# Performance work log

Measured on AMD Instinct MI355X. Metric: run time of the kernel, lower is better.

## Reference

```python
import jax, jax.numpy as jnp
import numpy as np

N_NODES = 50000
N_EDGES = 800000
IN_DIM = 128
ATT_DIM = 128
NEG_SLOPE = 0.01  # nn.LeakyReLU default


def setup_inputs() -> dict:
    key = jax.random.key(0)
    ks = jax.random.split(key, 8)
    x = jax.random.normal(ks[0], (N_NODES, IN_DIM), dtype=jnp.float32)
    src_idx = jax.random.randint(ks[1], (N_EDGES,), 0, N_NODES, dtype=jnp.int32)
    dst_idx = jax.random.randint(ks[2], (N_EDGES,), 0, N_NODES, dtype=jnp.int32)
    # small init scale keeps exp(score) numerically tame
    src_w = jax.random.normal(ks[3], (IN_DIM, ATT_DIM), dtype=jnp.float32) * 0.05
    src_b = jnp.zeros((ATT_DIM,), dtype=jnp.float32)
    dst_w = jax.random.normal(ks[4], (IN_DIM, ATT_DIM), dtype=jnp.float32) * 0.05
    dst_b = jnp.zeros((ATT_DIM,), dtype=jnp.float32)
    att_w = jax.random.normal(ks[5], (ATT_DIM, 1), dtype=jnp.float32) * 0.05
    att_b = jnp.zeros((1,), dtype=jnp.float32)
    return {"x": x, "src_idx": src_idx, "dst_idx": dst_idx,
            "src_w": src_w, "src_b": src_b, "dst_w": dst_w, "dst_b": dst_b,
            "att_w": att_w, "att_b": att_b}


def reference(x, src_idx, dst_idx, src_w, src_b, dst_w, dst_b, att_w, att_b):
    n = x.shape[0]
    # 1) mean aggregation of source features onto destinations (copy_u + mean)
    deg = jax.ops.segment_sum(jnp.ones_like(dst_idx, dtype=x.dtype), dst_idx, num_segments=n)
    h_mean = jax.ops.segment_sum(x[src_idx], dst_idx, num_segments=n)
    h_mean = h_mean / jnp.maximum(deg, 1.0)[:, None]
    # 2) attention projections on nodes (dense GEMMs)
    ha_src = x @ src_w + src_b          # [N, att_dim]
    ha_dst = h_mean @ dst_w + dst_b     # [N, att_dim]
    # 3) per-edge u_add_v -> LeakyReLU -> att Linear -> exp
    e = jax.nn.leaky_relu(ha_src[src_idx] + ha_dst[dst_idx], NEG_SLOPE)  # [E, att_dim]
    s = jnp.exp(e @ att_w + att_b)      # [E, 1]
    # 4) edge softmax: normalize by segment sum over destination
    denom = jax.ops.segment_sum(s, dst_idx, num_segments=n)  # [N, 1]
    a = s / denom[dst_idx]              # [E, 1]
    # 5) u_mul_e weighted aggregation (sum)
    out = jax.ops.segment_sum(x[src_idx] * a, dst_idx, num_segments=n)  # [N, in_dim]
    return out
```

## Files before the change

kernel.cpp:

```cpp
#include <hip/hip_runtime.h>
#include <math.h>

#define N_NODES 50000
#define N_EDGES 800000
#define DIM 128
#define NEG_SLOPE 0.01f
#define CAP 64
#define DEGS 32

#define GEMM_BLOCKS 3125
#define SCAT_BLOCKS 3125

typedef short v8s __attribute__((ext_vector_type(8)));
typedef float v4f __attribute__((ext_vector_type(4)));
typedef float v2f __attribute__((ext_vector_type(2)));

__device__ inline unsigned f2bf2(float a, float b) {
    unsigned ua = __float_as_uint(a);
    unsigned ub = __float_as_uint(b);
    ua = (ua + 0x7fffu + ((ua >> 16) & 1u)) >> 16;
    ub = (ub + 0x7fffu + ((ub >> 16) & 1u)) & 0xffff0000u;
    return ua | ub;
}
__device__ inline v2f bf2v(unsigned u) {
    v2f r;
    r.x = __uint_as_float(u << 16);
    r.y = __uint_as_float(u & 0xffff0000u);
    return r;
}
__device__ inline v2f lk2(v2f v) {
    return __builtin_elementwise_max(v, v * NEG_SLOPE);
}

#define ROR_ADD(v, CTRL) \
    ((v) + __int_as_float(__builtin_amdgcn_update_dpp( \
        0, __float_as_int(v), (CTRL), 0xf, 0xf, false)))

__global__ __launch_bounds__(256) void k_scatter(
    const int* __restrict__ src, const int* __restrict__ dst,
    int* __restrict__ deg, int* __restrict__ slots,
    const float* __restrict__ src_w, const float* __restrict__ dst_w,
    unsigned* __restrict__ whT)
{
    int bx = blockIdx.x;
    int tid = threadIdx.x;
    if (bx < 64) {
        int gid = bx * 256 + tid;
        int n = gid >> 6;
        int kk = gid & 63;
        const float* W = (n < 128) ? src_w : dst_w;
        int col = n & 127;
        float w0 = W[(2 * kk) * DIM + col];
        float w1 = W[(2 * kk + 1) * DIM + col];
        whT[gid] = f2bf2(w0, w1);
    }
    int e = bx * 256 + tid;
    int s = src[e];
    int d = dst[e];
    int pos = atomicAdd(&deg[d * DEGS], 1);
    if (pos < CAP) slots[d * CAP + pos] = s * 64;
}

__global__ __launch_bounds__(64) void k_gemm(
    const float* __restrict__ x, const unsigned* __restrict__ whT,
    const float* __restrict__ src_b, unsigned* __restrict__ hx_u,
    unsigned* __restrict__ yu)
{
    __shared__ unsigned L[16][132];
    int bx = blockIdx.x;
    int lane = threadIdx.x;
    int quad = lane >> 4;
    int m = lane & 15;

    int arow = bx * 16 + m;
    const float4* xp = (const float4*)(x + (size_t)arow * DIM + quad * 8);
    float4 f[4][2];
    #pragma unroll
    for (int k0 = 0; k0 < 4; ++k0) {
        f[k0][0] = xp[k0 * 8];
        f[k0][1] = xp[k0 * 8 + 1];
    }

    v8s b[4];
    #pragma unroll
    for (int k0 = 0; k0 < 4; ++k0) {
        union { unsigned u[4]; v8s s; } pk;
        pk.u[0] = f2bf2(f[k0][0].x, f[k0][0].y);
        pk.u[1] = f2bf2(f[k0][0].z, f[k0][0].w);
        pk.u[2] = f2bf2(f[k0][1].x, f[k0][1].y);
        pk.u[3] = f2bf2(f[k0][1].z, f[k0][1].w);
        b[k0] = pk.s;
        int c = k0 * 32 + quad * 8 + 1;
        L[m][c + 0] = pk.u[0];
        L[m][c + 2] = pk.u[1];
        L[m][c + 4] = pk.u[2];
        L[m][c + 6] = pk.u[3];
    }

    v4f yacc[8];
    #pragma unroll
    for (int nt = 0; nt < 16; ++nt) {
        v4f acc = {0.f, 0.f, 0.f, 0.f};
        const uint4* ap = (const uint4*)(whT + (size_t)(nt * 16 + m) * 64 + quad * 4);
        #pragma unroll
        for (int k0 = 0; k0 < 4; ++k0) {
            union { uint4 u; v8s s; } af;
            af.u = ap[k0 * 4];
            acc = __builtin_amdgcn_mfma_f32_16x16x32_bf16(af.s, b[k0], acc, 0, 0, 0);
        }
        if (nt < 8) {
            float4 bia = ((const float4*)src_b)[nt * 4 + quad];
            int c = nt * 16 + quad * 4;
            L[m][c]     = f2bf2(acc[0] + bia.x, acc[1] + bia.y);
            L[m][c + 2] = f2bf2(acc[2] + bia.z, acc[3] + bia.w);
        } else {
            yacc[nt - 8] = acc;
        }
    }

    int rbase0 = bx * 16;
    for (int i = lane; i < 512; i += 64) {
        int r = i >> 5, c = i & 31;
        ((uint4*)(hx_u + (size_t)(rbase0 + r) * 128))[c] = *(const uint4*)&L[r][c * 4];
    }

    #pragma unroll
    for (int t = 0; t < 8; ++t) {
        int c = t * 8 + quad * 2;
        L[m][c]     = f2bf2(yacc[t][0], yacc[t][1]);
        L[m][c + 1] = f2bf2(yacc[t][2], yacc[t][3]);
    }
    for (int i = lane; i < 256; i += 64) {
        int r = i >> 4, c = i & 15;
        ((uint4*)(yu + (size_t)(rbase0 + r) * 64))[c] = *(const uint4*)&L[r][c * 4];
    }
}

__global__ __launch_bounds__(256) void k_fuse(
    const uint2* __restrict__ hx, const unsigned* __restrict__ yu,
    const int* __restrict__ slots, const int* __restrict__ deg,
    const float* __restrict__ dst_b, const float* __restrict__ att_w,
    const float* __restrict__ att_b, float* __restrict__ out)
{
    int g = blockIdx.x * 256 + threadIdx.x;
    int node = g >> 6;
    int lane = g & 63;
    int grp = lane >> 4;
    int sl = lane & 15;
    int cnt = deg[node * DEGS];
    if (cnt == 0) {
        if (grp < 2) {
            v4f z = {0.f, 0.f, 0.f, 0.f};
            __builtin_nontemporal_store(z, (v4f*)out + node * 32 + (grp ? 16 + sl : sl));
        }
        return;
    }
    int cc = (cnt < CAP) ? cnt : CAP;
    int trips = (cc + 3) >> 2;
    int myoff = (lane < cc) ? slots[node * CAP + lane] : 0;

    v2f hd01 = {0.f, 0.f}, hd23 = {0.f, 0.f};
    v2f hd45 = {0.f, 0.f}, hd67 = {0.f, 0.f};
    #pragma unroll 4
    for (int t = 0; t < trips; ++t) {
        int i = 4 * t + grp;
        bool valid = (i < cc);
        int off = __shfl(myoff, valid ? i : 0);
        if (valid) {
            const uint2* yp = (const uint2*)(yu + off);
            uint2 qa = yp[sl];
            uint2 qb = yp[16 + sl];
            hd01 += bf2v(qa.x);
            hd23 += bf2v(qa.y);
            hd45 += bf2v(qb.x);
            hd67 += bf2v(qb.y);
        }
    }
    float inv = 1.0f / (float)cnt;
    float m0 = hd01.x, m1 = hd01.y, m2 = hd23.x, m3 = hd23.y;
    float m4 = hd45.x, m5 = hd45.y, m6 = hd67.x, m7 = hd67.y;
    #define XRED(f) { f += __shfl_xor(f, 32); f += __shfl_xor(f, 16); f *= inv; }
    XRED(m0) XRED(m1) XRED(m2) XRED(m3) XRED(m4) XRED(m5) XRED(m6) XRED(m7)
    #undef XRED
    float4 db0 = ((const float4*)dst_b)[sl];
    float4 db1 = ((const float4*)dst_b)[16 + sl];
    hd01 = (v2f){m0 + db0.x, m1 + db0.y};
    hd23 = (v2f){m2 + db0.z, m3 + db0.w};
    hd45 = (v2f){m4 + db1.x, m5 + db1.y};
    hd67 = (v2f){m6 + db1.z, m7 + db1.w};

    float4 aw0f = ((const float4*)att_w)[sl];
    float4 aw1f = ((const float4*)att_w)[16 + sl];
    v2f aw01 = (v2f){aw0f.x, aw0f.y}, aw23 = (v2f){aw0f.z, aw0f.w};
    v2f aw45 = (v2f){aw1f.x, aw1f.y}, aw67 = (v2f){aw1f.z, aw1f.w};
    float ab = att_b[0];
    v2f o01 = {0.f, 0.f}, o23 = {0.f, 0.f};
    v2f o45 = {0.f, 0.f}, o67 = {0.f, 0.f};
    float dsum = 0.f;
    #pragma unroll 4
    for (int t = 0; t < trips; ++t) {
        int i = 4 * t + grp;
        bool valid = (i < cc);
        int off = __shfl(myoff, valid ? i : 0);
        if (valid) {
            const uint4* hp = (const uint4*)(hx + off);
            uint4 qa = hp[sl];
            uint4 qb = hp[16 + sl];
            v2f p2 = {0.f, 0.f};
            p2 = __builtin_elementwise_fma(lk2(bf2v(qa.x) + hd01), aw01, p2);
            p2 = __builtin_elementwise_fma(lk2(bf2v(qa.z) + hd23), aw23, p2);
            p2 = __builtin_elementwise_fma(lk2(bf2v(qb.x) + hd45), aw45, p2);
            p2 = __builtin_elementwise_fma(lk2(bf2v(qb.z) + hd67), aw67, p2);
            float p = p2.x + p2.y;
            p = ROR_ADD(p, 0x128);
            p = ROR_ADD(p, 0x124);
            p = ROR_ADD(p, 0x122);
            p = ROR_ADD(p, 0x121);
            float s = __expf(p + ab);
            v2f s2 = (v2f){s, s};
            o01 = __builtin_elementwise_fma(bf2v(qa.y), s2, o01);
            o23 = __builtin_elementwise_fma(bf2v(qa.w), s2, o23);
            o45 = __builtin_elementwise_fma(bf2v(qb.y), s2, o45);
            o67 = __builtin_elementwise_fma(bf2v(qb.w), s2, o67);
            dsum += s;
        }
    }
    dsum += __shfl_xor(dsum, 32);
    dsum += __shfl_xor(dsum, 16);
    float r0 = o01.x, r1 = o01.y, r2 = o23.x, r3 = o23.y;
    float r4 = o45.x, r5 = o45.y, r6 = o67.x, r7 = o67.y;
    #define XRED2(f) { f += __shfl_xor(f, 32); f += __shfl_xor(f, 16); }
    XRED2(r0) XRED2(r1) XRED2(r2) XRED2(r3) XRED2(r4) XRED2(r5) XRED2(r6) XRED2(r7)
    #undef XRED2
    float r = 1.0f / dsum;
    if (grp < 2) {
        v4f ov;
        if (grp == 0) {
            ov[0] = r0 * r; ov[1] = r1 * r; ov[2] = r2 * r; ov[3] = r3 * r;
            __builtin_nontemporal_store(ov, (v4f*)out + node * 32 + sl);
        } else {
            ov[0] = r4 * r; ov[1] = r5 * r; ov[2] = r6 * r; ov[3] = r7 * r;
            __builtin_nontemporal_store(ov, (v4f*)out + node * 32 + 16 + sl);
        }
    }
}

extern "C" void kernel_launch(void* const* d_in, const int* in_sizes, int n_in,
                              void* d_out, int out_size, void* d_ws, size_t ws_size,
                              hipStream_t stream)
{
    const float* x     = (const float*)d_in[0];
    const int*   src   = (const int*)d_in[1];
    const int*   dst   = (const int*)d_in[2];
    const float* src_w = (const float*)d_in[3];
    const float* src_b = (const float*)d_in[4];
    const float* dst_w = (const float*)d_in[5];
    const float* dst_b = (const float*)d_in[6];
    const float* att_w = (const float*)d_in[7];
    const float* att_b = (const float*)d_in[8];
    float* out = (float*)d_out;
    (void)in_sizes; (void)n_in; (void)out_size; (void)ws_size;

    const size_t NF = (size_t)N_NODES * DIM;

    int* ws = (int*)d_ws;
    int* ideg  = ws;
    int* slots = ws + 1600512;
    unsigned* whT = (unsigned*)(ws + 4800512);
    unsigned* yu  = whT + 16384;
    uint2*    hx  = (uint2*)(yu + NF / 2);

    hipMemsetAsync(ideg, 0, (size_t)N_NODES * DEGS * sizeof(int), stream);

    k_scatter<<<SCAT_BLOCKS, 256, 0, stream>>>(
        src, dst, ideg, slots, src_w, dst_w, whT);

    k_gemm<<<GEMM_BLOCKS, 64, 0, stream>>>(x, whT, src_b, (unsigned*)hx, yu);

    k_fuse<<<N_NODES * 64 / 256, 256, 0, stream>>>(
        hx, yu, slots, ideg, dst_b, att_w, att_b, out);
}
```

Measured before the change: 246.8 us.

## Merge edge scatter into GEMM kernel and replace memset with prep kernel

Splits the weight transpose/bf16 pack into a small prep kernel that also zeroes the degree counters, which removes the hipMemsetAsync. The edge scatter and node GEMM now share one launch, with odd and even blocks interleaved so the atomic-heavy scatter overlaps the MFMA GEMM. Scatter blocks now run 64 threads handling 4 edges each. This saves a launch and lets the latency-bound atomics hide under compute, at the cost of smaller scatter blocks and a heterogeneous grid.

```diff
diff --git a/kernel.cpp b/kernel.cpp
--- a/kernel.cpp
+++ b/kernel.cpp
@@ -10,6 +10,7 @@
 
 #define GEMM_BLOCKS 3125
 #define SCAT_BLOCKS 3125
+#define MERGED_BLOCKS (GEMM_BLOCKS + SCAT_BLOCKS)
 
 typedef short v8s __attribute__((ext_vector_type(8)));
 typedef float v4f __attribute__((ext_vector_type(4)));
@@ -36,16 +37,12 @@
     ((v) + __int_as_float(__builtin_amdgcn_update_dpp( \
         0, __float_as_int(v), (CTRL), 0xf, 0xf, false)))
 
-__global__ __launch_bounds__(256) void k_scatter(
-    const int* __restrict__ src, const int* __restrict__ dst,
-    int* __restrict__ deg, int* __restrict__ slots,
+__global__ __launch_bounds__(256) void k_prepw(
     const float* __restrict__ src_w, const float* __restrict__ dst_w,
-    unsigned* __restrict__ whT)
-{
-    int bx = blockIdx.x;
-    int tid = threadIdx.x;
-    if (bx < 64) {
-        int gid = bx * 256 + tid;
+    unsigned* __restrict__ whT, int* __restrict__ deg)
+{
+    int gid = blockIdx.x * 256 + threadIdx.x;
+    if (gid < 256 * 64) {
         int n = gid >> 6;
         int kk = gid & 63;
         const float* W = (n < 128) ? src_w : dst_w;
@@ -54,21 +51,39 @@
         float w1 = W[(2 * kk + 1) * DIM + col];
         whT[gid] = f2bf2(w0, w1);
     }
-    int e = bx * 256 + tid;
-    int s = src[e];
-    int d = dst[e];
-    int pos = atomicAdd(&deg[d * DEGS], 1);
-    if (pos < CAP) slots[d * CAP + pos] = s * 64;
-}
-
-__global__ __launch_bounds__(64) void k_gemm(
+    if (gid < N_NODES) deg[gid * DEGS] = 0;
+}
+
+__global__ __launch_bounds__(64) void k_scatgemm(
+    const int* __restrict__ src, const int* __restrict__ dst,
+    int* __restrict__ deg, int* __restrict__ slots,
     const float* __restrict__ x, const unsigned* __restrict__ whT,
     const float* __restrict__ src_b, unsigned* __restrict__ hx_u,
     unsigned* __restrict__ yu)
 {
     __shared__ unsigned L[16][132];
-    int bx = blockIdx.x;
+    int b = blockIdx.x;
     int lane = threadIdx.x;
+
+    if (b & 1) {
+        int bs = b >> 1;
+        int e0 = bs * 256 + lane;
+        int sv[4], dv[4], pos[4];
+        #pragma unroll
+        for (int i = 0; i < 4; ++i) {
+            sv[i] = src[e0 + i * 64];
+            dv[i] = dst[e0 + i * 64];
+        }
+        #pragma unroll
+        for (int i = 0; i < 4; ++i)
+            pos[i] = atomicAdd(&deg[dv[i] * DEGS], 1);
+        #pragma unroll
+        for (int i = 0; i < 4; ++i)
+            if (pos[i] < CAP) slots[dv[i] * CAP + pos[i]] = sv[i] * 64;
+        return;
+    }
+
+    int bx = b >> 1;
     int quad = lane >> 4;
     int m = lane & 15;
 
@@ -81,7 +96,7 @@
         f[k0][1] = xp[k0 * 8 + 1];
     }
 
-    v8s b[4];
+    v8s bb[4];
     #pragma unroll
     for (int k0 = 0; k0 < 4; ++k0) {
         union { unsigned u[4]; v8s s; } pk;
@@ -89,7 +104,7 @@
         pk.u[1] = f2bf2(f[k0][0].z, f[k0][0].w);
         pk.u[2] = f2bf2(f[k0][1].x, f[k0][1].y);
         pk.u[3] = f2bf2(f[k0][1].z, f[k0][1].w);
-        b[k0] = pk.s;
+        bb[k0] = pk.s;
         int c = k0 * 32 + quad * 8 + 1;
         L[m][c + 0] = pk.u[0];
         L[m][c + 2] = pk.u[1];
@@ -106,7 +121,7 @@
         for (int k0 = 0; k0 < 4; ++k0) {
             union { uint4 u; v8s s; } af;
             af.u = ap[k0 * 4];
-            acc = __builtin_amdgcn_mfma_f32_16x16x32_bf16(af.s, b[k0], acc, 0, 0, 0);
+            acc = __builtin_amdgcn_mfma_f32_16x16x32_bf16(af.s, bb[k0], acc, 0, 0, 0);
         }
         if (nt < 8) {
             float4 bia = ((const float4*)src_b)[nt * 4 + quad];
@@ -270,12 +285,10 @@
     unsigned* yu  = whT + 16384;
     uint2*    hx  = (uint2*)(yu + NF / 2);
 
-    hipMemsetAsync(ideg, 0, (size_t)N_NODES * DEGS * sizeof(int), stream);
-
-    k_scatter<<<SCAT_BLOCKS, 256, 0, stream>>>(
-        src, dst, ideg, slots, src_w, dst_w, whT);
-
-    k_gemm<<<GEMM_BLOCKS, 64, 0, stream>>>(x, whT, src_b, (unsigned*)hx, yu);
+    k_prepw<<<256, 256, 0, stream>>>(src_w, dst_w, whT, ideg);
+
+    k_scatgemm<<<MERGED_BLOCKS, 64, 0, stream>>>(
+        src, dst, ideg, slots, x, whT, src_b, (unsigned*)hx, yu);
 
     k_fuse<<<N_NODES * 64 / 256, 256, 0, stream>>>(
         hx, yu, slots, ideg, dst_b, att_w, att_b, out);
```

After: 242.0 us. Within noise of the previous version (-1.9%).
